# Kernel optimization log

Measured on AMD Instinct MI355X. Metric: run time of the kernel, lower is better.

Reference implementation:

```python
import jax, jax.numpy as jnp
import numpy as np

B, T, D = 16, 512, 256
HH = D // 2   # per-direction hidden of bidirectional GRU
G, Z, R, NA = 32, 8, 16, 18


def _gru_step(h, x, wih, whh, bih, bhh):
    # torch.nn.GRUCell math
    gi = x @ wih.T + bih
    gh = h @ whh.T + bhh
    ir, iz, inn = jnp.split(gi, 3, axis=-1)
    hr, hz, hn = jnp.split(gh, 3, axis=-1)
    r = jax.nn.sigmoid(ir + hr)
    z = jax.nn.sigmoid(iz + hz)
    n = jnp.tanh(inn + r * hn)
    return (1.0 - z) * n + z * h


def _gru_seq(x_tbd, wih, whh, bih, bhh):
    h0 = jnp.zeros((x_tbd.shape[1], whh.shape[1]), x_tbd.dtype)
    def step(h, x):
        h = _gru_step(h, x, wih, whh, bih, bhh)
        return h, h
    _, hs = jax.lax.scan(step, h0, x_tbd)
    return hs  # (T, B, H)


def setup_inputs() -> dict:
    key = jax.random.key(0)
    ks = jax.random.split(key, 26)
    rn = lambda k, s, sc: jax.random.normal(k, s, jnp.float32) * sc
    d = {
        'e_seq': rn(ks[0], (B, T, D), 1.0),
        'eps':   rn(ks[1], (B, T, Z), 1.0),
        # acausal bidirectional GRU (fwd + bwd cells)
        'wih_f': rn(ks[2], (3 * HH, D), D ** -0.5),  'whh_f': rn(ks[3], (3 * HH, HH), HH ** -0.5),
        'bih_f': jnp.zeros((3 * HH,)), 'bhh_f': jnp.zeros((3 * HH,)),
        'wih_b': rn(ks[4], (3 * HH, D), D ** -0.5),  'whh_b': rn(ks[5], (3 * HH, HH), HH ** -0.5),
        'bih_b': jnp.zeros((3 * HH,)), 'bhh_b': jnp.zeros((3 * HH,)),
        # controller encoder GRUCell(2D -> G) + heads
        'wih_e': rn(ks[6], (3 * G, 2 * D), (2 * D) ** -0.5), 'whh_e': rn(ks[7], (3 * G, G), G ** -0.5),
        'bih_e': jnp.zeros((3 * G,)), 'bhh_e': jnp.zeros((3 * G,)),
        'mu_w': rn(ks[8], (Z, G), G ** -0.5),  'mu_b': jnp.zeros((Z,)),
        'lv_w': rn(ks[9], (Z, G), G ** -0.5),  'lv_b': jnp.zeros((Z,)),
        # switching unit MLP (D+G+Z -> 64 -> 1)
        'sw1_w': rn(ks[10], (64, D + G + Z), (D + G + Z) ** -0.5), 'sw1_b': jnp.zeros((64,)),
        'sw2_w': rn(ks[11], (1, 64), 64 ** -0.5), 'sw2_b': jnp.zeros((1,)),
        # decoder hypernet (Z -> 32 -> 2*D*R)
        'dec1_w': rn(ks[12], (32, Z), Z ** -0.5), 'dec1_b': jnp.zeros((32,)),
        'dec2_w': rn(ks[13], (2 * D * R, 32), 32 ** -0.5), 'dec2_b': jnp.zeros((2 * D * R,)),
        # final norm + action head
        'ln_g': jnp.ones((D,)), 'ln_b': jnp.zeros((D,)),
        'head_w': rn(ks[14], (NA, D), D ** -0.5), 'head_b': jnp.zeros((NA,)),
    }
    return d


def _forward(e_seq, eps, wih_f, whh_f, bih_f, bhh_f, wih_b, whh_b, bih_b, bhh_b,
             wih_e, whh_e, bih_e, bhh_e, mu_w, mu_b, lv_w, lv_b,
             sw1_w, sw1_b, sw2_w, sw2_b, dec1_w, dec1_b, dec2_w, dec2_b,
             ln_g, ln_b, head_w, head_b):
    Bz, Tt, Dm = e_seq.shape
    e_tbd = jnp.swapaxes(e_seq, 0, 1)                      # (T, B, D)
    # AcausalEmbedder: bidirectional GRU
    fwd = _gru_seq(e_tbd, wih_f, whh_f, bih_f, bhh_f)
    bwd = _gru_seq(e_tbd[::-1], wih_b, whh_b, bih_b, bhh_b)[::-1]
    s_tbd = jnp.concatenate([fwd, bwd], axis=-1)           # (T, B, D)
    eps_tbd = jnp.swapaxes(eps, 0, 1)

    h0 = jnp.zeros((Bz, whh_e.shape[1]), e_seq.dtype)
    z0 = jnp.zeros((Bz, mu_w.shape[0]), e_seq.dtype)

    def step(carry, xs):
        h, z_prev = carry
        e_t, s_t, eps_t = xs
        h = _gru_step(h, jnp.concatenate([e_t, s_t], axis=-1), wih_e, whh_e, bih_e, bhh_e)
        mu = h @ mu_w.T + mu_b
        logvar = h @ lv_w.T + lv_b
        # switching unit uses updated h (causal)
        hid = jnp.tanh(jnp.concatenate([e_t, h, z_prev], axis=-1) @ sw1_w.T + sw1_b)
        beta = jax.nn.sigmoid(hid @ sw2_w.T + sw2_b)       # (B, 1)
        z = beta * (mu + jnp.exp(0.5 * logvar) * eps_t) + (1.0 - beta) * z_prev
        return (h, jax.lax.stop_gradient(z)), (mu, logvar, beta, z)

    _, (mu_t, lv_t, be_t, z_t) = jax.lax.scan(step, (h0, z0), (e_tbd, s_tbd, eps_tbd))
    mu_seq = jnp.swapaxes(mu_t, 0, 1)
    logvar_seq = jnp.swapaxes(lv_t, 0, 1)
    beta_seq = jnp.swapaxes(be_t, 0, 1)
    z_seq = jnp.swapaxes(z_t, 0, 1)                        # (B, T, Z)

    # ControllerDecoder: z -> (A, Bm); apply U = A @ Bm^T without materializing U
    hmid = jnp.tanh(z_seq @ dec1_w.T + dec1_b)
    ab = hmid @ dec2_w.T + dec2_b                          # (B, T, 2*D*R)
    DR = ab.shape[-1] // 2
    A = ab[..., :DR].reshape(Bz, Tt, Dm, -1)               # (B, T, D, R)
    Bm = ab[..., DR:].reshape(Bz, Tt, Dm, -1)
    tmp = jnp.einsum('btdr,btd->btr', Bm, e_seq)
    perturbed = e_seq + jnp.einsum('btdr,btr->btd', A, tmp)

    # final LayerNorm + action head on obs positions
    mean = perturbed.mean(-1, keepdims=True)
    var = perturbed.var(-1, keepdims=True)
    xn = (perturbed - mean) * jax.lax.rsqrt(var + 1e-5) * ln_g + ln_b
    logits = xn @ head_w.T + head_b                        # (B, T, NA)
    return logits, mu_seq, logvar_seq, beta_seq, z_seq


def reference(e_seq, eps, wih_f, whh_f, bih_f, bhh_f, wih_b, whh_b, bih_b, bhh_b,
              wih_e, whh_e, bih_e, bhh_e, mu_w, mu_b, lv_w, lv_b,
              sw1_w, sw1_b, sw2_w, sw2_b, dec1_w, dec1_b, dec2_w, dec2_b,
              ln_g, ln_b, head_w, head_b):
    return _forward(e_seq, eps, wih_f, whh_f, bih_f, bhh_f, wih_b, whh_b, bih_b, bhh_b,
                    wih_e, whh_e, bih_e, bhh_e, mu_w, mu_b, lv_w, lv_b,
                    sw1_w, sw1_b, sw2_w, sw2_b, dec1_w, dec1_b, dec2_w, dec2_b,
                    ln_g, ln_b, head_w, head_b)
```

## Files before the change

kernel.cpp:

```cpp
#include <hip/hip_runtime.h>

#define TT 512
#define BB 16
#define DD 256
#define HHH 128
#define GG 32
#define ZZ 8
#define RR_ 16
#define NAA 18

typedef _Float16 h2v __attribute__((ext_vector_type(2)));
typedef __attribute__((ext_vector_type(4))) float f4;
typedef __attribute__((ext_vector_type(4))) int i4;

__device__ __forceinline__ float sigmoid_(float x) { return 1.f / (1.f + __expf(-x)); }
__device__ __forceinline__ float tanh_(float x) { float e = __expf(2.f * x); return 1.f - 2.f / (e + 1.f); }
__device__ __forceinline__ float dot4(float4 a, float4 b) {
    return a.x * b.x + a.y * b.y + a.z * b.z + a.w * b.w;
}
__device__ __forceinline__ h2v u2h2(unsigned u) { union { unsigned u; h2v h; } c; c.u = u; return c.h; }

__device__ __forceinline__ void lds_barrier() {
    asm volatile("s_waitcnt lgkmcnt(0)" ::: "memory");
    __builtin_amdgcn_s_barrier();
}

#define AGPR_STORE(a, v) asm volatile("v_accvgpr_write_b32 %0, %1" : "=a"(a) : "v"(v))
#define AGPR_LOAD(v, a)  asm volatile("v_accvgpr_read_b32 %0, %1" : "=v"(v) : "a"(a))

template <int CTRL, int RM, int BM, bool BC>
__device__ __forceinline__ float dpp_add_f(float v) {
    return v + __int_as_float(__builtin_amdgcn_update_dpp(0, __float_as_int(v), CTRL, RM, BM, BC));
}
__device__ __forceinline__ float wave_sum_bcast(float p) {
    p = dpp_add_f<0x111, 0xf, 0xf, true>(p);
    p = dpp_add_f<0x112, 0xf, 0xf, true>(p);
    p = dpp_add_f<0x114, 0xf, 0xf, true>(p);
    p = dpp_add_f<0x118, 0xf, 0xf, true>(p);
    p = dpp_add_f<0x142, 0xa, 0xf, false>(p);
    p = dpp_add_f<0x143, 0xc, 0xf, false>(p);
    return __int_as_float(__builtin_amdgcn_readlane(__float_as_int(p), 63));
}
__device__ __forceinline__ float quad_sum(float v) {
    v = dpp_add_f<0xB1, 0xf, 0xf, true>(v);
    v = dpp_add_f<0x4E, 0xf, 0xf, true>(v);
    return v;
}

__global__ __launch_bounds__(256) void pack_w(
    const float* __restrict__ wf, const float* __restrict__ wb,
    const float* __restrict__ we,
    unsigned* __restrict__ pk, unsigned* __restrict__ pk_e)
{
    int i = blockIdx.x * 256 + threadIdx.x;
    if (i < 49152) {
        int dir = i / 24576; int r = i % 24576;
        int w = r / 3072;    int r2 = r % 3072;
        int T = r2 / 1024;   int r3 = r2 % 1024;
        int kt = r3 / 256;   int r4 = r3 % 256;
        int lane = r4 / 4;   int jd = r4 % 4;
        const float* wsrc = dir ? wb : wf;
        int row = T * 128 + 16 * w + (lane & 15);
        int k0 = kt * 32 + (lane >> 4) * 8 + 2 * jd;
        union { _Float16 h[2]; unsigned u; } c;
        c.h[0] = (_Float16)wsrc[row * 128 + k0];
        c.h[1] = (_Float16)wsrc[row * 128 + k0 + 1];
        pk[i] = c.u;
    } else if (i < 50688) {
        int ie = i - 49152;
        int s = ie / 384;  int rem = ie % 384;
        int k = rem / 12;  int e = rem % 12;
        int j = e / 4;     int m = e % 4;
        int row = j * 32 + k, k0 = 8 * s + 2 * m;
        union { _Float16 h[2]; unsigned u; } c;
        c.h[0] = (_Float16)we[row * 32 + k0];
        c.h[1] = (_Float16)we[row * 32 + k0 + 1];
        pk_e[ie] = c.u;
    }
}

__global__ __launch_bounds__(256) void gemm_k(
    const float* __restrict__ A, int K, const float* __restrict__ W, int ldw,
    const float* __restrict__ bias, float* __restrict__ Out, int ldout, int N, int accFlag)
{
    __shared__ float At[64][36];
    __shared__ float Wt[32][36];
    int row0 = blockIdx.x * 64, n0 = blockIdx.y * 32;
    int tid = threadIdx.x;
    int tx = tid & 15, ty = tid >> 4;
    float acc[4][2] = {};
    for (int k0 = 0; k0 < K; k0 += 32) {
        #pragma unroll
        for (int i = 0; i < 8; ++i) {
            int idx = tid + i * 256; int rr = idx >> 5, kk = idx & 31;
            At[rr][kk] = A[(size_t)(row0 + rr) * K + k0 + kk];
        }
        #pragma unroll
        for (int i = 0; i < 4; ++i) {
            int idx = tid + i * 256; int nn = idx >> 5, kk = idx & 31;
            Wt[nn][kk] = (n0 + nn < N) ? W[(size_t)(n0 + nn) * ldw + k0 + kk] : 0.f;
        }
        __syncthreads();
        #pragma unroll
        for (int kk = 0; kk < 32; kk += 4) {
            float4 w0 = *(const float4*)&Wt[tx][kk];
            float4 w1 = *(const float4*)&Wt[tx + 16][kk];
            #pragma unroll
            for (int rr = 0; rr < 4; ++rr) {
                float4 av = *(const float4*)&At[ty * 4 + rr][kk];
                acc[rr][0] += dot4(av, w0);
                acc[rr][1] += dot4(av, w1);
            }
        }
        __syncthreads();
    }
    #pragma unroll
    for (int cc = 0; cc < 2; ++cc) {
        int n = n0 + tx + cc * 16;
        if (n < N) {
            float badd = bias ? bias[n] : 0.f;
            #pragma unroll
            for (int rr = 0; rr < 4; ++rr) {
                int row = row0 + ty * 4 + rr;
                float v = acc[rr][cc] + badd;
                if (accFlag) Out[(size_t)row * ldout + n] += v;
                else         Out[(size_t)row * ldout + n] = v;
            }
        }
    }
}

__global__ __launch_bounds__(256) void gemm_gi(
    const float* __restrict__ A,
    const float* __restrict__ wf, const float* __restrict__ bf, float* __restrict__ of,
    const float* __restrict__ wb, const float* __restrict__ bb, float* __restrict__ ob)
{
    __shared__ float At[64][36];
    __shared__ float Wt[32][36];
    int y = blockIdx.y;
    const float* W; const float* bias; float* Out; int n0;
    if (y < 12) { W = wf; bias = bf; Out = of; n0 = y * 32; }
    else        { W = wb; bias = bb; Out = ob; n0 = (y - 12) * 32; }
    int row0 = blockIdx.x * 64;
    int tid = threadIdx.x;
    int tx = tid & 15, ty = tid >> 4;
    float acc[4][2] = {};
    for (int k0 = 0; k0 < 256; k0 += 32) {
        #pragma unroll
        for (int i = 0; i < 8; ++i) {
            int idx = tid + i * 256; int rr = idx >> 5, kk = idx & 31;
            At[rr][kk] = A[(size_t)(row0 + rr) * 256 + k0 + kk];
        }
        #pragma unroll
        for (int i = 0; i < 4; ++i) {
            int idx = tid + i * 256; int nn = idx >> 5, kk = idx & 31;
            Wt[nn][kk] = W[(size_t)(n0 + nn) * 256 + k0 + kk];
        }
        __syncthreads();
        #pragma unroll
        for (int kk = 0; kk < 32; kk += 4) {
            float4 w0 = *(const float4*)&Wt[tx][kk];
            float4 w1 = *(const float4*)&Wt[tx + 16][kk];
            #pragma unroll
            for (int rr = 0; rr < 4; ++rr) {
                float4 av = *(const float4*)&At[ty * 4 + rr][kk];
                acc[rr][0] += dot4(av, w0);
                acc[rr][1] += dot4(av, w1);
            }
        }
        __syncthreads();
    }
    #pragma unroll
    for (int cc = 0; cc < 2; ++cc) {
        int n = n0 + tx + cc * 16;
        float badd = bias[n];
        #pragma unroll
        for (int rr = 0; rr < 4; ++rr) {
            int row = row0 + ty * 4 + rr;
            Out[(size_t)row * 384 + n] = acc[rr][cc] + badd;
        }
    }
}

struct __align__(16) SmGru { _Float16 hb[2][128]; };
struct __align__(16) SmGemm { float At[64][36]; float Wt[32][36]; };
union __align__(16) SmU { SmGru g; SmGemm m; };

__device__ __forceinline__ void gemm_tile512(
    const float* __restrict__ A, int K, const float* __restrict__ W, int ldw,
    const float* __restrict__ bias, float* __restrict__ Out, int ldout, int N,
    int row0, int n0, SmGemm& sm)
{
    int tid = threadIdx.x;
    int tx = tid & 31, ty = tid >> 5;
    float acc[4] = {};
    for (int k0 = 0; k0 < K; k0 += 32) {
        #pragma unroll
        for (int i = 0; i < 4; ++i) {
            int idx = tid + i * 512; int rr = idx >> 5, kk = idx & 31;
            sm.At[rr][kk] = A[(size_t)(row0 + rr) * K + k0 + kk];
        }
        #pragma unroll
        for (int i = 0; i < 2; ++i) {
            int idx = tid + i * 512; int nn = idx >> 5, kk = idx & 31;
            sm.Wt[nn][kk] = (n0 + nn < N) ? W[(size_t)(n0 + nn) * ldw + k0 + kk] : 0.f;
        }
        __syncthreads();
        #pragma unroll
        for (int kk = 0; kk < 32; kk += 4) {
            float4 w0 = *(const float4*)&sm.Wt[tx][kk];
            #pragma unroll
            for (int rr = 0; rr < 4; ++rr) {
                float4 av = *(const float4*)&sm.At[ty * 4 + rr][kk];
                acc[rr] += dot4(av, w0);
            }
        }
        __syncthreads();
    }
    int n = n0 + tx;
    if (n < N) {
        float badd = bias ? bias[n] : 0.f;
        #pragma unroll
        for (int rr = 0; rr < 4; ++rr)
            Out[(size_t)(row0 + ty * 4 + rr) * ldout + n] = acc[rr] + badd;
    }
}

__global__ __launch_bounds__(512, 2) void gru_fused(
    const float* __restrict__ gi_f, const float* __restrict__ gi_b,
    const unsigned* __restrict__ pk,
    const float* __restrict__ bhh_f, const float* __restrict__ bhh_b,
    float* __restrict__ s_seq,
    const float* __restrict__ e,
    const float* __restrict__ wih_e, const float* __restrict__ bih_e, float* __restrict__ gie,
    const float* __restrict__ sw1_w, const float* __restrict__ sw1_b, float* __restrict__ swe)
{
    __shared__ SmU sm;
    int bx = blockIdx.x;
    if (bx >= 416) {
        int t = bx - 416;
        gemm_tile512(e, 256, sw1_w, 296, sw1_b, swe, 64, 64, (t & 127) * 64, (t >> 7) * 32, sm.m);
        return;
    }
    if (bx >= 32) {
        int t = bx - 32;
        gemm_tile512(e, 256, wih_e, 512, bih_e, gie, 96, 96, (t & 127) * 64, (t >> 7) * 32, sm.m);
        return;
    }

    int dir = bx >> 4, b = bx & 15;
    const float* gi  = dir ? gi_b  : gi_f;
    const float* bhh = dir ? bhh_b : bhh_f;
    int tid = threadIdx.x;
    int w = tid >> 6;
    int lane = tid & 63;
    int quad = lane >> 4;
    int c = lane & 15;
    int j = 16 * w + c;

    i4 bf[3][4];
    #pragma unroll
    for (int T = 0; T < 3; ++T)
        #pragma unroll
        for (int kt = 0; kt < 4; ++kt)
            bf[T][kt] = *(const i4*)(pk + (size_t)((((dir * 8 + w) * 3 + T) * 4 + kt) * 64 + lane) * 4);
    #pragma unroll
    for (int T = 0; T < 3; ++T)
        #pragma unroll
        for (int kt = 0; kt < 4; ++kt)
            asm volatile("" : "+a"(bf[T][kt]));

    if (tid < 128) sm.g.hb[0][tid] = (_Float16)0.f;

    float bhr = 0.f, bhz = 0.f, bhn = 0.f;
    float gra = 0.f, gza = 0.f, gna = 0.f;
    float grb = 0.f, gzb = 0.f, gnb = 0.f;
    float hreg = 0.f;
    if (lane < 16) {
        bhr = bhh[j]; bhz = bhh[128 + j]; bhn = bhh[256 + j];
        int t0 = dir ? 511 : 0;
        int t1 = dir ? 510 : 1;
        size_t p0 = (size_t)(b * TT + t0) * 384;
        size_t p1 = (size_t)(b * TT + t1) * 384;
        gra = gi[p0 + j]; gza = gi[p0 + 128 + j]; gna = gi[p0 + 256 + j];
        grb = gi[p1 + j]; gzb = gi[p1 + 128 + j]; gnb = gi[p1 + 256 + j];
    }
    __syncthreads();

    int cur = 0;
    auto body = [&](int step, float& gr, float& gz, float& gn) {
        i4 af[4];
        #pragma unroll
        for (int kt = 0; kt < 4; ++kt)
            af[kt] = *(const i4*)(&sm.g.hb[cur][kt * 32 + quad * 8]);
        f4 accr = {0.f, 0.f, 0.f, 0.f};
        f4 accz = {0.f, 0.f, 0.f, 0.f};
        f4 accn = {0.f, 0.f, 0.f, 0.f};
        asm volatile("s_nop 3");
        #pragma unroll
        for (int kt = 0; kt < 4; ++kt) {
            asm volatile("v_mfma_f32_16x16x32_f16 %0, %1, %2, %0" : "+v"(accr) : "v"(af[kt]), "a"(bf[0][kt]));
            asm volatile("v_mfma_f32_16x16x32_f16 %0, %1, %2, %0" : "+v"(accz) : "v"(af[kt]), "a"(bf[1][kt]));
            asm volatile("v_mfma_f32_16x16x32_f16 %0, %1, %2, %0" : "+v"(accn) : "v"(af[kt]), "a"(bf[2][kt]));
        }
        asm volatile("s_nop 7\n\ts_nop 7");
        if (lane < 16) {
            int t = dir ? (511 - step) : step;
            int p = b * TT + t;
            float r = sigmoid_(gr + bhr + accr[0]);
            float z = sigmoid_(gz + bhz + accz[0]);
            float n = tanh_(gn + r * (bhn + accn[0]));
            float hn = (1.f - z) * n + z * hreg;
            hreg = hn;
            sm.g.hb[cur ^ 1][j] = (_Float16)hn;
            s_seq[(size_t)p * 256 + dir * 128 + j] = hn;
            int s2 = step + 2;
            int tp = (s2 < 512) ? (dir ? (511 - s2) : s2) : t;
            size_t p2 = (size_t)(b * TT + tp) * 384;
            gr = gi[p2 + j]; gz = gi[p2 + 128 + j]; gn = gi[p2 + 256 + j];
        }
        lds_barrier();
        cur ^= 1;
    };

    for (int step = 0; step < 512; step += 2) {
        body(step,     gra, gza, gna);
        body(step + 1, grb, gzb, gnb);
    }
}

__global__ __launch_bounds__(256) void heads_k(
    const float* __restrict__ h_seq,
    const float* __restrict__ mu_w, const float* __restrict__ mu_b,
    const float* __restrict__ lv_w, const float* __restrict__ lv_b,
    const float* __restrict__ sw1_w,
    float* __restrict__ out_mu, float* __restrict__ out_lv, float* __restrict__ swe)
{
    __shared__ __align__(16) float Ah[64][32];
    int row0 = blockIdx.x * 64;
    int tid = threadIdx.x;
    #pragma unroll
    for (int i = 0; i < 8; ++i) {
        int idx = tid + i * 256; int rr = idx >> 5, kk = idx & 31;
        Ah[rr][kk] = h_seq[(size_t)(row0 + rr) * 32 + kk];
    }
    __syncthreads();
    int r = tid >> 2, g = tid & 3;
    const float4* av = (const float4*)Ah[r];
    float4 a[8];
    #pragma unroll
    for (int i = 0; i < 8; ++i) a[i] = av[i];
    int row = row0 + r;
    for (int c = 0; c < 20; ++c) {
        int n = g * 20 + c;
        const float* wrow;
        if (n < 8)       wrow = mu_w + n * 32;
        else if (n < 16) wrow = lv_w + (n - 8) * 32;
        else             wrow = sw1_w + (size_t)(n - 16) * 296 + 256;
        const float4* wv = (const float4*)wrow;
        float acc = 0.f;
        #pragma unroll
        for (int i = 0; i < 8; ++i) acc += dot4(wv[i], a[i]);
        if (n < 8)       out_mu[row * 8 + n] = acc + mu_b[n];
        else if (n < 16) out_lv[row * 8 + (n - 8)] = acc + lv_b[n - 8];
        else             swe[(size_t)row * 64 + (n - 16)] += acc;
    }
}

__global__ __launch_bounds__(128, 1) void ctrl_h_scan(
    const float* __restrict__ gie, const unsigned* __restrict__ pk_e,
    const float* __restrict__ bhh_e, float* __restrict__ h_seq)
{
    int b = blockIdx.x, tid = threadIdx.x;
    int k = tid >> 2;
    int s = tid & 3;

    unsigned ag[12];
    {
        const uint4* wp = (const uint4*)(pk_e + ((size_t)(s * 32) + k) * 12);
        #pragma unroll
        for (int i = 0; i < 3; ++i) {
            uint4 u = wp[i];
            AGPR_STORE(ag[4 * i + 0], u.x);
            AGPR_STORE(ag[4 * i + 1], u.y);
            AGPR_STORE(ag[4 * i + 2], u.z);
            AGPR_STORE(ag[4 * i + 3], u.w);
        }
    }

    __shared__ __align__(16) _Float16 hb[2][32];
    if (tid < 32) hb[0][tid] = (_Float16)0.f;

    int pbase = b * TT;
    float bhr = 0.f, bhz = 0.f, bhn = 0.f;
    float g1a = 0.f, g2a = 0.f, g3a = 0.f, g1b = 0.f, g2b = 0.f, g3b = 0.f;
    float hreg = 0.f;
    if (s == 0) {
        bhr = bhh_e[k]; bhz = bhh_e[32 + k]; bhn = bhh_e[64 + k];
        size_t p0 = (size_t)pbase * 96, p1 = (size_t)(pbase + 1) * 96;
        g1a = gie[p0 + k]; g2a = gie[p0 + 32 + k]; g3a = gie[p0 + 64 + k];
        g1b = gie[p1 + k]; g2b = gie[p1 + 32 + k]; g3b = gie[p1 + 64 + k];
    }
    __syncthreads();

    int cur = 0;
    auto body = [&](int t, float& g1, float& g2, float& g3) {
        const uint4* hv = (const uint4*)(&hb[cur][0]) + s;
        uint4 h4 = hv[0];
        unsigned hw[4] = { h4.x, h4.y, h4.z, h4.w };
        float a0 = 0.f, a1 = 0.f, a2 = 0.f;
        #pragma unroll
        for (int m = 0; m < 4; ++m) {
            unsigned w0, w1, w2;
            AGPR_LOAD(w0, ag[m]);
            AGPR_LOAD(w1, ag[4 + m]);
            AGPR_LOAD(w2, ag[8 + m]);
            h2v hh = u2h2(hw[m]);
            a0 = __builtin_amdgcn_fdot2(u2h2(w0), hh, a0, false);
            a1 = __builtin_amdgcn_fdot2(u2h2(w1), hh, a1, false);
            a2 = __builtin_amdgcn_fdot2(u2h2(w2), hh, a2, false);
        }
        a0 = quad_sum(a0);
        a1 = quad_sum(a1);
        a2 = quad_sum(a2);

        if (s == 0) {
            float r = sigmoid_(g1 + bhr + a0);
            float z = sigmoid_(g2 + bhz + a1);
            float n = tanh_(g3 + r * (bhn + a2));
            float hn = (1.f - z) * n + z * hreg;
            hreg = hn;
            hb[cur ^ 1][k] = (_Float16)hn;
            h_seq[(size_t)(pbase + t) * 32 + k] = hn;
            int t2 = (t + 2 < 512) ? t + 2 : t;
            size_t p2 = (size_t)(pbase + t2) * 96;
            g1 = gie[p2 + k]; g2 = gie[p2 + 32 + k]; g3 = gie[p2 + 64 + k];
        }
        lds_barrier();
        cur ^= 1;
    };

    for (int t = 0; t < 512; t += 2) {
        body(t,     g1a, g2a, g3a);
        body(t + 1, g1b, g2b, g3b);
    }
}

__global__ __launch_bounds__(64, 1) void ctrl_z_scan(
    const float* __restrict__ hid_pre, const float* __restrict__ sw1_w,
    const float* __restrict__ sw2_w, const float* __restrict__ sw2_b,
    const float* __restrict__ eps, const float* __restrict__ mu_o,
    const float* __restrict__ lv_o, float* __restrict__ beta_o, float* __restrict__ z_o)
{
    int b = blockIdx.x, q = threadIdx.x;
    float wz[8];
    #pragma unroll
    for (int x = 0; x < 8; ++x) wz[x] = sw1_w[(size_t)q * 296 + 288 + x];
    float w2 = sw2_w[q];
    float bb = sw2_b[0];
    float4 z03 = {0.f, 0.f, 0.f, 0.f}, z47 = {0.f, 0.f, 0.f, 0.f};
    int pbase = b * TT;

    auto loadcand = [&](int p, float4& c03, float4& c47) {
        float4 m0 = *(const float4*)(mu_o + p * 8);
        float4 m1 = *(const float4*)(mu_o + p * 8 + 4);
        float4 l0 = *(const float4*)(lv_o + p * 8);
        float4 l1 = *(const float4*)(lv_o + p * 8 + 4);
        float4 e0 = *(const float4*)(eps + p * 8);
        float4 e1 = *(const float4*)(eps + p * 8 + 4);
        c03 = make_float4(m0.x + __expf(0.5f * l0.x) * e0.x, m0.y + __expf(0.5f * l0.y) * e0.y,
                          m0.z + __expf(0.5f * l0.z) * e0.z, m0.w + __expf(0.5f * l0.w) * e0.w);
        c47 = make_float4(m1.x + __expf(0.5f * l1.x) * e1.x, m1.y + __expf(0.5f * l1.y) * e1.y,
                          m1.z + __expf(0.5f * l1.z) * e1.z, m1.w + __expf(0.5f * l1.w) * e1.w);
    };

    float hpa = hid_pre[(size_t)pbase * 64 + q];
    float hpb = hid_pre[(size_t)(pbase + 1) * 64 + q];
    float4 c03a, c47a, c03b, c47b;
    loadcand(pbase, c03a, c47a);
    loadcand(pbase + 1, c03b, c47b);

    auto body = [&](int t, float& hp, float4& c03, float4& c47) {
        int p = pbase + t;
        float a = hp
            + wz[0] * z03.x + wz[1] * z03.y + wz[2] * z03.z + wz[3] * z03.w
            + wz[4] * z47.x + wz[5] * z47.y + wz[6] * z47.z + wz[7] * z47.w;
        float hid = tanh_(a);
        float total = wave_sum_bcast(w2 * hid);
        float beta = sigmoid_(total + bb);
        float omb = 1.f - beta;
        z03.x = beta * c03.x + omb * z03.x;  z03.y = beta * c03.y + omb * z03.y;
        z03.z = beta * c03.z + omb * z03.z;  z03.w = beta * c03.w + omb * z03.w;
        z47.x = beta * c47.x + omb * z47.x;  z47.y = beta * c47.y + omb * z47.y;
        z47.z = beta * c47.z + omb * z47.z;  z47.w = beta * c47.w + omb * z47.w;
        if (q == 0) {
            *(float4*)(z_o + p * 8) = z03;
            *(float4*)(z_o + p * 8 + 4) = z47;
            beta_o[p] = beta;
        }
        int t2 = (t + 2 < 512) ? t + 2 : t;
        hp = hid_pre[(size_t)(pbase + t2) * 64 + q];
        loadcand(pbase + t2, c03, c47);
    };

    for (int t = 0; t < 512; t += 2) {
        body(t,     hpa, c03a, c47a);
        body(t + 1, hpb, c03b, c47b);
    }
}

__global__ __launch_bounds__(256, 3) void decoder_final(
    const float* __restrict__ e_seq, const float* __restrict__ z_o,
    const float* __restrict__ dec1_w, const float* __restrict__ dec1_b,
    const float* __restrict__ dec2_w, const float* __restrict__ dec2_b,
    const float* __restrict__ ln_g, const float* __restrict__ ln_b,
    const float* __restrict__ head_w, const float* __restrict__ head_b,
    float* __restrict__ logits)
{
    __shared__ __align__(16) float e_l[8][256];
    __shared__ __align__(16) float hmid[8][32];
    __shared__ float zl[8][8];
    __shared__ float tmpw[8][16];
    __shared__ __align__(16) float partb[2048];
    __shared__ float red1[8][16];
    __shared__ float red2[8][16];
    __shared__ float stats[8][2];
    int tid = threadIdx.x;
    int p0 = blockIdx.x * 8;

    {
        const float4* eg = (const float4*)(e_seq + (size_t)p0 * 256);
        float4* el4 = (float4*)&e_l[0][0];
        el4[tid] = eg[tid];
        el4[tid + 256] = eg[tid + 256];
        if (tid < 64) ((float*)zl)[tid] = z_o[p0 * 8 + tid];
    }
    __syncthreads();
    {
        int pp = tid >> 5, g = tid & 31;
        float a = dec1_b[g];
        #pragma unroll
        for (int x = 0; x < 8; ++x) a += dec1_w[g * 8 + x] * zl[pp][x];
        hmid[pp][g] = tanh_(a);
    }
    __syncthreads();
    {
        int r = tid & 15, dgrp = tid >> 4;
        float acc[8];
        #pragma unroll
        for (int pp = 0; pp < 8; ++pp) acc[pp] = 0.f;
        for (int iblk = 0; iblk < 8; ++iblk) {
            float4 wr[2][8]; float wb[2]; int dd[2];
            #pragma unroll
            for (int ii = 0; ii < 2; ++ii) {
                int d = dgrp + 16 * (iblk * 2 + ii);
                dd[ii] = d;
                int row = 4096 + d * 16 + r;
                const float4* wp = (const float4*)(dec2_w + (size_t)row * 32);
                #pragma unroll
                for (int g = 0; g < 8; ++g) wr[ii][g] = wp[g];
                wb[ii] = dec2_b[row];
            }
            #pragma unroll 1
            for (int pp = 0; pp < 8; ++pp) {
                const float4* hv = (const float4*)hmid[pp];
                float b0 = wb[0], b1 = wb[1];
                #pragma unroll
                for (int g = 0; g < 8; ++g) {
                    float4 hh = hv[g];
                    b0 += dot4(wr[0][g], hh);
                    b1 += dot4(wr[1][g], hh);
                }
                acc[pp] += b0 * e_l[pp][dd[0]] + b1 * e_l[pp][dd[1]];
            }
        }
        #pragma unroll
        for (int pp = 0; pp < 8; ++pp) partb[(pp * 16 + r) * 16 + dgrp] = acc[pp];
    }
    __syncthreads();
    if (tid < 128) {
        int pp = tid >> 4, rr = tid & 15;
        float s = 0.f;
        #pragma unroll
        for (int dg = 0; dg < 16; ++dg) s += partb[(pp * 16 + rr) * 16 + dg];
        tmpw[pp][rr] = s;
    }
    __syncthreads();
    {
        int d = tid;
        float po[8];
        #pragma unroll
        for (int pp = 0; pp < 8; ++pp) po[pp] = e_l[pp][d];
        for (int rblk = 0; rblk < 8; ++rblk) {
            float4 wr[2][8]; float wb[2];
            #pragma unroll
            for (int ii = 0; ii < 2; ++ii) {
                int row = d * 16 + rblk * 2 + ii;
                const float4* wp = (const float4*)(dec2_w + (size_t)row * 32);
                #pragma unroll
                for (int g = 0; g < 8; ++g) wr[ii][g] = wp[g];
                wb[ii] = dec2_b[row];
            }
            #pragma unroll 1
            for (int pp = 0; pp < 8; ++pp) {
                const float4* hv = (const float4*)hmid[pp];
                float a0 = wb[0], a1 = wb[1];
                #pragma unroll
                for (int g = 0; g < 8; ++g) {
                    float4 hh = hv[g];
                    a0 += dot4(wr[0][g], hh);
                    a1 += dot4(wr[1][g], hh);
                }
                po[pp] += a0 * tmpw[pp][rblk * 2] + a1 * tmpw[pp][rblk * 2 + 1];
            }
        }
        #pragma unroll
        for (int pp = 0; pp < 8; ++pp) partb[pp * 256 + d] = po[pp];
    }
    __syncthreads();
    if (tid < 128) {
        int pp = tid >> 4, c = tid & 15;
        float s = 0.f, s2 = 0.f;
        #pragma unroll
        for (int i = 0; i < 16; ++i) { float v = partb[pp * 256 + c * 16 + i]; s += v; s2 += v * v; }
        red1[pp][c] = s; red2[pp][c] = s2;
    }
    __syncthreads();
    if (tid < 8) {
        float s = 0.f, s2 = 0.f;
        #pragma unroll
        for (int c = 0; c < 16; ++c) { s += red1[tid][c]; s2 += red2[tid][c]; }
        float mean = s * (1.f / 256.f);
        float var = s2 * (1.f / 256.f) - mean * mean;
        stats[tid][0] = mean;
        stats[tid][1] = rsqrtf(var + 1e-5f);
    }
    __syncthreads();
    {
        int d = tid;
        float g = ln_g[d], bln = ln_b[d];
        #pragma unroll
        for (int pp = 0; pp < 8; ++pp) {
            float v = (partb[pp * 256 + d] - stats[pp][0]) * stats[pp][1];
            partb[pp * 256 + d] = v * g + bln;
        }
    }
    __syncthreads();
    if (tid < 144) {
        int pp = tid / 18, na = tid - pp * 18;
        float a = head_b[na];
        for (int d2 = 0; d2 < 256; ++d2)
            a += partb[pp * 256 + d2] * head_w[na * 256 + d2];
        logits[(size_t)(p0 + pp) * 18 + na] = a;
    }
}

extern "C" void kernel_launch(void* const* d_in, const int* in_sizes, int n_in,
                              void* d_out, int out_size, void* d_ws, size_t ws_size,
                              hipStream_t stream) {
    (void)in_sizes; (void)n_in; (void)out_size; (void)ws_size;
    const float* e     = (const float*)d_in[0];
    const float* eps   = (const float*)d_in[1];
    const float* wih_f = (const float*)d_in[2];
    const float* whh_f = (const float*)d_in[3];
    const float* bih_f = (const float*)d_in[4];
    const float* bhh_f = (const float*)d_in[5];
    const float* wih_b = (const float*)d_in[6];
    const float* whh_b = (const float*)d_in[7];
    const float* bih_b = (const float*)d_in[8];
    const float* bhh_b = (const float*)d_in[9];
    const float* wih_e = (const float*)d_in[10];
    const float* whh_e = (const float*)d_in[11];
    const float* bih_e = (const float*)d_in[12];
    const float* bhh_e = (const float*)d_in[13];
    const float* mu_w  = (const float*)d_in[14];
    const float* mu_b  = (const float*)d_in[15];
    const float* lv_w  = (const float*)d_in[16];
    const float* lv_b  = (const float*)d_in[17];
    const float* sw1_w = (const float*)d_in[18];
    const float* sw1_b = (const float*)d_in[19];
    const float* sw2_w = (const float*)d_in[20];
    const float* sw2_b = (const float*)d_in[21];
    const float* dec1_w = (const float*)d_in[22];
    const float* dec1_b = (const float*)d_in[23];
    const float* dec2_w = (const float*)d_in[24];
    const float* dec2_b = (const float*)d_in[25];
    const float* ln_g  = (const float*)d_in[26];
    const float* ln_b  = (const float*)d_in[27];
    const float* head_w = (const float*)d_in[28];
    const float* head_b = (const float*)d_in[29];

    float* ws    = (float*)d_ws;
    float* gi_f  = ws;
    float* gi_b  = gi_f + 3145728;
    float* gie   = gi_b + 3145728;
    float* swe   = gie + 786432;
    float* s_seq = swe + 524288;
    float* h_seq = s_seq + 2097152;
    unsigned* pk   = (unsigned*)(h_seq + 262144);
    unsigned* pk_e = pk + 49152;

    float* out       = (float*)d_out;
    float* out_logit = out;
    float* out_mu    = out + 147456;
    float* out_lv    = out + 212992;
    float* out_beta  = out + 278528;
    float* out_z     = out + 286720;

    pack_w<<<198, 256, 0, stream>>>(whh_f, whh_b, whh_e, pk, pk_e);
    gemm_gi<<<dim3(128, 24), 256, 0, stream>>>(e, wih_f, bih_f, gi_f, wih_b, bih_b, gi_b);
    gru_fused<<<672, 512, 0, stream>>>(gi_f, gi_b, pk, bhh_f, bhh_b, s_seq,
                                       e, wih_e, bih_e, gie, sw1_w, sw1_b, swe);
    gemm_k<<<dim3(128, 3), 256, 0, stream>>>(s_seq, 256, wih_e + 256, 512, nullptr, gie, 96, 96, 1);
    ctrl_h_scan<<<16, 128, 0, stream>>>(gie, pk_e, bhh_e, h_seq);
    heads_k<<<128, 256, 0, stream>>>(h_seq, mu_w, mu_b, lv_w, lv_b, sw1_w, out_mu, out_lv, swe);
    ctrl_z_scan<<<16, 64, 0, stream>>>(swe, sw1_w, sw2_w, sw2_b, eps, out_mu, out_lv, out_beta, out_z);
    decoder_final<<<1024, 256, 0, stream>>>(e, out_z, dec1_w, dec1_b, dec2_w, dec2_b,
                                            ln_g, ln_b, head_w, head_b, out_logit);
}
```

Before: 1.097 ms.

## Fuse controller GRU scan, heads and switch scan into one pipelined kernel

Replaces the separate ctrl_h_scan, heads_k and ctrl_z_scan launches with one kernel per batch row. Wave 0 runs the controller GRU recurrence and wave 1 runs the mu/logvar heads and the switching z-scan one step behind, passing h through LDS, so the two serial scans overlap and the h_seq round trip through global memory goes away. The bidirectional GRU MFMA chain is also split into two independent accumulator chains so consecutive MFMAs do not wait on each other. The costs are more per-thread registers and a barrier every step between the two waves.

```diff
diff --git a/kernel.cpp b/kernel.cpp
--- a/kernel.cpp
+++ b/kernel.cpp
@@ -24,9 +24,6 @@
     asm volatile("s_waitcnt lgkmcnt(0)" ::: "memory");
     __builtin_amdgcn_s_barrier();
 }
-
-#define AGPR_STORE(a, v) asm volatile("v_accvgpr_write_b32 %0, %1" : "=a"(a) : "v"(v))
-#define AGPR_LOAD(v, a)  asm volatile("v_accvgpr_read_b32 %0, %1" : "=v"(v) : "a"(a))
 
 template <int CTRL, int RM, int BM, bool BC>
 __device__ __forceinline__ float dpp_add_f(float v) {
@@ -293,23 +290,32 @@
         #pragma unroll
         for (int kt = 0; kt < 4; ++kt)
             af[kt] = *(const i4*)(&sm.g.hb[cur][kt * 32 + quad * 8]);
-        f4 accr = {0.f, 0.f, 0.f, 0.f};
-        f4 accz = {0.f, 0.f, 0.f, 0.f};
-        f4 accn = {0.f, 0.f, 0.f, 0.f};
+        f4 accrA = {0.f, 0.f, 0.f, 0.f}, accrB = {0.f, 0.f, 0.f, 0.f};
+        f4 acczA = {0.f, 0.f, 0.f, 0.f}, acczB = {0.f, 0.f, 0.f, 0.f};
+        f4 accnA = {0.f, 0.f, 0.f, 0.f}, accnB = {0.f, 0.f, 0.f, 0.f};
         asm volatile("s_nop 3");
-        #pragma unroll
-        for (int kt = 0; kt < 4; ++kt) {
-            asm volatile("v_mfma_f32_16x16x32_f16 %0, %1, %2, %0" : "+v"(accr) : "v"(af[kt]), "a"(bf[0][kt]));
-            asm volatile("v_mfma_f32_16x16x32_f16 %0, %1, %2, %0" : "+v"(accz) : "v"(af[kt]), "a"(bf[1][kt]));
-            asm volatile("v_mfma_f32_16x16x32_f16 %0, %1, %2, %0" : "+v"(accn) : "v"(af[kt]), "a"(bf[2][kt]));
-        }
+        asm volatile("v_mfma_f32_16x16x32_f16 %0, %1, %2, %0" : "+v"(accrA) : "v"(af[0]), "a"(bf[0][0]));
+        asm volatile("v_mfma_f32_16x16x32_f16 %0, %1, %2, %0" : "+v"(acczA) : "v"(af[0]), "a"(bf[1][0]));
+        asm volatile("v_mfma_f32_16x16x32_f16 %0, %1, %2, %0" : "+v"(accnA) : "v"(af[0]), "a"(bf[2][0]));
+        asm volatile("v_mfma_f32_16x16x32_f16 %0, %1, %2, %0" : "+v"(accrB) : "v"(af[2]), "a"(bf[0][2]));
+        asm volatile("v_mfma_f32_16x16x32_f16 %0, %1, %2, %0" : "+v"(acczB) : "v"(af[2]), "a"(bf[1][2]));
+        asm volatile("v_mfma_f32_16x16x32_f16 %0, %1, %2, %0" : "+v"(accnB) : "v"(af[2]), "a"(bf[2][2]));
+        asm volatile("v_mfma_f32_16x16x32_f16 %0, %1, %2, %0" : "+v"(accrA) : "v"(af[1]), "a"(bf[0][1]));
+        asm volatile("v_mfma_f32_16x16x32_f16 %0, %1, %2, %0" : "+v"(acczA) : "v"(af[1]), "a"(bf[1][1]));
+        asm volatile("v_mfma_f32_16x16x32_f16 %0, %1, %2, %0" : "+v"(accnA) : "v"(af[1]), "a"(bf[2][1]));
+        asm volatile("v_mfma_f32_16x16x32_f16 %0, %1, %2, %0" : "+v"(accrB) : "v"(af[3]), "a"(bf[0][3]));
+        asm volatile("v_mfma_f32_16x16x32_f16 %0, %1, %2, %0" : "+v"(acczB) : "v"(af[3]), "a"(bf[1][3]));
+        asm volatile("v_mfma_f32_16x16x32_f16 %0, %1, %2, %0" : "+v"(accnB) : "v"(af[3]), "a"(bf[2][3]));
         asm volatile("s_nop 7\n\ts_nop 7");
         if (lane < 16) {
             int t = dir ? (511 - step) : step;
             int p = b * TT + t;
-            float r = sigmoid_(gr + bhr + accr[0]);
-            float z = sigmoid_(gz + bhz + accz[0]);
-            float n = tanh_(gn + r * (bhn + accn[0]));
+            float ar = accrA[0] + accrB[0];
+            float az = acczA[0] + acczB[0];
+            float an = accnA[0] + accnB[0];
+            float r = sigmoid_(gr + bhr + ar);
+            float z = sigmoid_(gz + bhz + az);
+            float n = tanh_(gn + r * (bhn + an));
             float hn = (1.f - z) * n + z * hreg;
             hreg = hn;
             sm.g.hb[cur ^ 1][j] = (_Float16)hn;
@@ -329,184 +335,172 @@
     }
 }
 
-__global__ __launch_bounds__(256) void heads_k(
-    const float* __restrict__ h_seq,
+__global__ __launch_bounds__(128, 1) void ctrl_fused(
+    const float* __restrict__ gie, const unsigned* __restrict__ pk_e,
+    const float* __restrict__ bhh_e,
     const float* __restrict__ mu_w, const float* __restrict__ mu_b,
     const float* __restrict__ lv_w, const float* __restrict__ lv_b,
-    const float* __restrict__ sw1_w,
-    float* __restrict__ out_mu, float* __restrict__ out_lv, float* __restrict__ swe)
+    const float* __restrict__ sw1_w, const float* __restrict__ sw2_w,
+    const float* __restrict__ sw2_b,
+    const float* __restrict__ swe,
+    const float* __restrict__ eps,
+    float* __restrict__ out_mu, float* __restrict__ out_lv,
+    float* __restrict__ beta_o, float* __restrict__ z_o)
 {
-    __shared__ __align__(16) float Ah[64][32];
-    int row0 = blockIdx.x * 64;
+    int b = blockIdx.x;
     int tid = threadIdx.x;
-    #pragma unroll
-    for (int i = 0; i < 8; ++i) {
-        int idx = tid + i * 256; int rr = idx >> 5, kk = idx & 31;
-        Ah[rr][kk] = h_seq[(size_t)(row0 + rr) * 32 + kk];
-    }
-    __syncthreads();
-    int r = tid >> 2, g = tid & 3;
-    const float4* av = (const float4*)Ah[r];
-    float4 a[8];
-    #pragma unroll
-    for (int i = 0; i < 8; ++i) a[i] = av[i];
-    int row = row0 + r;
-    for (int c = 0; c < 20; ++c) {
-        int n = g * 20 + c;
-        const float* wrow;
-        if (n < 8)       wrow = mu_w + n * 32;
-        else if (n < 16) wrow = lv_w + (n - 8) * 32;
-        else             wrow = sw1_w + (size_t)(n - 16) * 296 + 256;
-        const float4* wv = (const float4*)wrow;
-        float acc = 0.f;
-        #pragma unroll
-        for (int i = 0; i < 8; ++i) acc += dot4(wv[i], a[i]);
-        if (n < 8)       out_mu[row * 8 + n] = acc + mu_b[n];
-        else if (n < 16) out_lv[row * 8 + (n - 8)] = acc + lv_b[n - 8];
-        else             swe[(size_t)row * 64 + (n - 16)] += acc;
-    }
-}
-
-__global__ __launch_bounds__(128, 1) void ctrl_h_scan(
-    const float* __restrict__ gie, const unsigned* __restrict__ pk_e,
-    const float* __restrict__ bhh_e, float* __restrict__ h_seq)
-{
-    int b = blockIdx.x, tid = threadIdx.x;
-    int k = tid >> 2;
-    int s = tid & 3;
-
-    unsigned ag[12];
-    {
-        const uint4* wp = (const uint4*)(pk_e + ((size_t)(s * 32) + k) * 12);
-        #pragma unroll
-        for (int i = 0; i < 3; ++i) {
-            uint4 u = wp[i];
-            AGPR_STORE(ag[4 * i + 0], u.x);
-            AGPR_STORE(ag[4 * i + 1], u.y);
-            AGPR_STORE(ag[4 * i + 2], u.z);
-            AGPR_STORE(ag[4 * i + 3], u.w);
-        }
-    }
+    int wid = tid >> 6;
+    int lane = tid & 63;
+    int pbase = b * TT;
 
     __shared__ __align__(16) _Float16 hb[2][32];
-    if (tid < 32) hb[0][tid] = (_Float16)0.f;
-
-    int pbase = b * TT;
-    float bhr = 0.f, bhz = 0.f, bhn = 0.f;
+    __shared__ __align__(16) float    hf[2][32];
+    __shared__ __align__(16) float    zc[8];
+
+    int k = lane >> 1, s2 = lane & 1;
+    unsigned wg[24];
+    float bhr = 0.f, bhz = 0.f, bhn = 0.f, hreg = 0.f;
     float g1a = 0.f, g2a = 0.f, g3a = 0.f, g1b = 0.f, g2b = 0.f, g3b = 0.f;
-    float hreg = 0.f;
-    if (s == 0) {
-        bhr = bhh_e[k]; bhz = bhh_e[32 + k]; bhn = bhh_e[64 + k];
-        size_t p0 = (size_t)pbase * 96, p1 = (size_t)(pbase + 1) * 96;
-        g1a = gie[p0 + k]; g2a = gie[p0 + 32 + k]; g3a = gie[p0 + 64 + k];
-        g1b = gie[p1 + k]; g2b = gie[p1 + 32 + k]; g3b = gie[p1 + 64 + k];
+    if (wid == 0) {
+        #pragma unroll
+        for (int ss = 0; ss < 2; ++ss) {
+            const uint4* wp = (const uint4*)(pk_e + ((size_t)((2 * s2 + ss) * 32) + k) * 12);
+            #pragma unroll
+            for (int i = 0; i < 3; ++i) {
+                uint4 u = wp[i];
+                wg[12 * ss + 4 * i + 0] = u.x;
+                wg[12 * ss + 4 * i + 1] = u.y;
+                wg[12 * ss + 4 * i + 2] = u.z;
+                wg[12 * ss + 4 * i + 3] = u.w;
+            }
+        }
+        if (tid < 32) hb[0][tid] = (_Float16)0.f;
+        if (s2 == 0) {
+            bhr = bhh_e[k]; bhz = bhh_e[32 + k]; bhn = bhh_e[64 + k];
+            size_t p0 = (size_t)pbase * 96, p1 = (size_t)(pbase + 1) * 96;
+            g1a = gie[p0 + k]; g2a = gie[p0 + 32 + k]; g3a = gie[p0 + 64 + k];
+            g1b = gie[p1 + k]; g2b = gie[p1 + 32 + k]; g3b = gie[p1 + 64 + k];
+        }
+    }
+
+    int q = lane;
+    int x = lane >> 3, kind = (lane >> 2) & 1, s = lane & 3;
+    float swh[32], wz[8], mlw[8];
+    float w2 = 0.f, sb2 = 0.f, mlb = 0.f;
+    float zreg[8] = {0.f, 0.f, 0.f, 0.f, 0.f, 0.f, 0.f, 0.f};
+    float hpa = 0.f, hpb = 0.f, epa = 0.f, epb = 0.f;
+    if (wid == 1) {
+        #pragma unroll
+        for (int kk = 0; kk < 32; ++kk) swh[kk] = sw1_w[(size_t)q * 296 + 256 + kk];
+        #pragma unroll
+        for (int xx = 0; xx < 8; ++xx) wz[xx] = sw1_w[(size_t)q * 296 + 288 + xx];
+        w2 = sw2_w[q];
+        sb2 = sw2_b[0];
+        const float* mw = kind ? lv_w : mu_w;
+        #pragma unroll
+        for (int m = 0; m < 8; ++m) mlw[m] = mw[x * 32 + 8 * s + m];
+        mlb = kind ? lv_b[x] : mu_b[x];
+        hpa = swe[(size_t)pbase * 64 + q];
+        hpb = swe[(size_t)(pbase + 1) * 64 + q];
+        epa = eps[(size_t)pbase * 8 + x];
+        epb = eps[(size_t)(pbase + 1) * 8 + x];
     }
     __syncthreads();
 
     int cur = 0;
-    auto body = [&](int t, float& g1, float& g2, float& g3) {
-        const uint4* hv = (const uint4*)(&hb[cur][0]) + s;
-        uint4 h4 = hv[0];
-        unsigned hw[4] = { h4.x, h4.y, h4.z, h4.w };
-        float a0 = 0.f, a1 = 0.f, a2 = 0.f;
+
+    auto prod = [&](int t, float& g1, float& g2, float& g3) {
+        const uint4* hv = (const uint4*)(&hb[cur][16 * s2]);
+        uint4 hA = hv[0], hB = hv[1];
+        unsigned hw[8] = {hA.x, hA.y, hA.z, hA.w, hB.x, hB.y, hB.z, hB.w};
+        float a0 = 0.f, a1 = 0.f, a2 = 0.f, c0 = 0.f, c1 = 0.f, c2 = 0.f;
         #pragma unroll
         for (int m = 0; m < 4; ++m) {
-            unsigned w0, w1, w2;
-            AGPR_LOAD(w0, ag[m]);
-            AGPR_LOAD(w1, ag[4 + m]);
-            AGPR_LOAD(w2, ag[8 + m]);
-            h2v hh = u2h2(hw[m]);
-            a0 = __builtin_amdgcn_fdot2(u2h2(w0), hh, a0, false);
-            a1 = __builtin_amdgcn_fdot2(u2h2(w1), hh, a1, false);
-            a2 = __builtin_amdgcn_fdot2(u2h2(w2), hh, a2, false);
-        }
-        a0 = quad_sum(a0);
-        a1 = quad_sum(a1);
-        a2 = quad_sum(a2);
-
-        if (s == 0) {
+            a0 = __builtin_amdgcn_fdot2(u2h2(wg[m]),      u2h2(hw[m]),     a0, false);
+            a1 = __builtin_amdgcn_fdot2(u2h2(wg[4 + m]),  u2h2(hw[m]),     a1, false);
+            a2 = __builtin_amdgcn_fdot2(u2h2(wg[8 + m]),  u2h2(hw[m]),     a2, false);
+            c0 = __builtin_amdgcn_fdot2(u2h2(wg[12 + m]), u2h2(hw[4 + m]), c0, false);
+            c1 = __builtin_amdgcn_fdot2(u2h2(wg[16 + m]), u2h2(hw[4 + m]), c1, false);
+            c2 = __builtin_amdgcn_fdot2(u2h2(wg[20 + m]), u2h2(hw[4 + m]), c2, false);
+        }
+        a0 += c0; a1 += c1; a2 += c2;
+        a0 = dpp_add_f<0xB1, 0xf, 0xf, true>(a0);
+        a1 = dpp_add_f<0xB1, 0xf, 0xf, true>(a1);
+        a2 = dpp_add_f<0xB1, 0xf, 0xf, true>(a2);
+        if (s2 == 0) {
             float r = sigmoid_(g1 + bhr + a0);
             float z = sigmoid_(g2 + bhz + a1);
             float n = tanh_(g3 + r * (bhn + a2));
             float hn = (1.f - z) * n + z * hreg;
             hreg = hn;
             hb[cur ^ 1][k] = (_Float16)hn;
-            h_seq[(size_t)(pbase + t) * 32 + k] = hn;
+            hf[cur ^ 1][k] = hn;
             int t2 = (t + 2 < 512) ? t + 2 : t;
             size_t p2 = (size_t)(pbase + t2) * 96;
             g1 = gie[p2 + k]; g2 = gie[p2 + 32 + k]; g3 = gie[p2 + 64 + k];
         }
+    };
+
+    auto cons = [&](int t, float& hp, float& ep) {
+        const float4* hv4 = (const float4*)(&hf[cur][0]);
+        float4 h4[8];
+        #pragma unroll
+        for (int i = 0; i < 8; ++i) h4[i] = hv4[i];
+        float a = hp;
+        #pragma unroll
+        for (int xx = 0; xx < 8; ++xx) a += wz[xx] * zreg[xx];
+        #pragma unroll
+        for (int i = 0; i < 8; ++i) {
+            a += swh[4 * i]     * h4[i].x;
+            a += swh[4 * i + 1] * h4[i].y;
+            a += swh[4 * i + 2] * h4[i].z;
+            a += swh[4 * i + 3] * h4[i].w;
+        }
+        float hid = tanh_(a);
+        float beta = sigmoid_(wave_sum_bcast(w2 * hid) + sb2);
+        float4 hs0 = *(const float4*)(&hf[cur][8 * s]);
+        float4 hs1 = *(const float4*)(&hf[cur][8 * s + 4]);
+        float pacc = mlw[0] * hs0.x + mlw[1] * hs0.y + mlw[2] * hs0.z + mlw[3] * hs0.w
+                   + mlw[4] * hs1.x + mlw[5] * hs1.y + mlw[6] * hs1.z + mlw[7] * hs1.w;
+        pacc = quad_sum(pacc);
+        float v = pacc + mlb;
+        float other = __int_as_float(__builtin_amdgcn_ds_swizzle(__float_as_int(v), 0x101F));
+        float muv = kind ? other : v;
+        float lvv = kind ? v : other;
+        float cand = muv + __expf(0.5f * lvv) * ep;
+        if ((lane & 7) == 0) zc[x] = cand;
+        asm volatile("s_waitcnt lgkmcnt(0)" ::: "memory");
+        float4 cz0 = *(const float4*)&zc[0];
+        float4 cz1 = *(const float4*)&zc[4];
+        float omb = 1.f - beta;
+        zreg[0] = beta * cz0.x + omb * zreg[0]; zreg[1] = beta * cz0.y + omb * zreg[1];
+        zreg[2] = beta * cz0.z + omb * zreg[2]; zreg[3] = beta * cz0.w + omb * zreg[3];
+        zreg[4] = beta * cz1.x + omb * zreg[4]; zreg[5] = beta * cz1.y + omb * zreg[5];
+        zreg[6] = beta * cz1.z + omb * zreg[6]; zreg[7] = beta * cz1.w + omb * zreg[7];
+        int p = pbase + t;
+        if (lane == 0) {
+            beta_o[p] = beta;
+            *(float4*)(z_o + (size_t)p * 8)     = make_float4(zreg[0], zreg[1], zreg[2], zreg[3]);
+            *(float4*)(z_o + (size_t)p * 8 + 4) = make_float4(zreg[4], zreg[5], zreg[6], zreg[7]);
+        }
+        if ((lane & 7) == 0) out_mu[(size_t)p * 8 + x] = muv;
+        if ((lane & 7) == 4) out_lv[(size_t)p * 8 + x] = lvv;
+        int t2 = (t + 2 < 512) ? t + 2 : t;
+        hp = swe[(size_t)(pbase + t2) * 64 + q];
+        ep = eps[(size_t)(pbase + t2) * 8 + x];
+    };
+
+    for (int it = 0; it < 512; it += 2) {
+        if (wid == 0) prod(it, g1a, g2a, g3a);
+        else if (it > 0) cons(it - 1, hpb, epb);
         lds_barrier();
         cur ^= 1;
-    };
-
-    for (int t = 0; t < 512; t += 2) {
-        body(t,     g1a, g2a, g3a);
-        body(t + 1, g1b, g2b, g3b);
-    }
-}
-
-__global__ __launch_bounds__(64, 1) void ctrl_z_scan(
-    const float* __restrict__ hid_pre, const float* __restrict__ sw1_w,
-    const float* __restrict__ sw2_w, const float* __restrict__ sw2_b,
-    const float* __restrict__ eps, const float* __restrict__ mu_o,
-    const float* __restrict__ lv_o, float* __restrict__ beta_o, float* __restrict__ z_o)
-{
-    int b = blockIdx.x, q = threadIdx.x;
-    float wz[8];
-    #pragma unroll
-    for (int x = 0; x < 8; ++x) wz[x] = sw1_w[(size_t)q * 296 + 288 + x];
-    float w2 = sw2_w[q];
-    float bb = sw2_b[0];
-    float4 z03 = {0.f, 0.f, 0.f, 0.f}, z47 = {0.f, 0.f, 0.f, 0.f};
-    int pbase = b * TT;
-
-    auto loadcand = [&](int p, float4& c03, float4& c47) {
-        float4 m0 = *(const float4*)(mu_o + p * 8);
-        float4 m1 = *(const float4*)(mu_o + p * 8 + 4);
-        float4 l0 = *(const float4*)(lv_o + p * 8);
-        float4 l1 = *(const float4*)(lv_o + p * 8 + 4);
-        float4 e0 = *(const float4*)(eps + p * 8);
-        float4 e1 = *(const float4*)(eps + p * 8 + 4);
-        c03 = make_float4(m0.x + __expf(0.5f * l0.x) * e0.x, m0.y + __expf(0.5f * l0.y) * e0.y,
-                          m0.z + __expf(0.5f * l0.z) * e0.z, m0.w + __expf(0.5f * l0.w) * e0.w);
-        c47 = make_float4(m1.x + __expf(0.5f * l1.x) * e1.x, m1.y + __expf(0.5f * l1.y) * e1.y,
-                          m1.z + __expf(0.5f * l1.z) * e1.z, m1.w + __expf(0.5f * l1.w) * e1.w);
-    };
-
-    float hpa = hid_pre[(size_t)pbase * 64 + q];
-    float hpb = hid_pre[(size_t)(pbase + 1) * 64 + q];
-    float4 c03a, c47a, c03b, c47b;
-    loadcand(pbase, c03a, c47a);
-    loadcand(pbase + 1, c03b, c47b);
-
-    auto body = [&](int t, float& hp, float4& c03, float4& c47) {
-        int p = pbase + t;
-        float a = hp
-            + wz[0] * z03.x + wz[1] * z03.y + wz[2] * z03.z + wz[3] * z03.w
-            + wz[4] * z47.x + wz[5] * z47.y + wz[6] * z47.z + wz[7] * z47.w;
-        float hid = tanh_(a);
-        float total = wave_sum_bcast(w2 * hid);
-        float beta = sigmoid_(total + bb);
-        float omb = 1.f - beta;
-        z03.x = beta * c03.x + omb * z03.x;  z03.y = beta * c03.y + omb * z03.y;
-        z03.z = beta * c03.z + omb * z03.z;  z03.w = beta * c03.w + omb * z03.w;
-        z47.x = beta * c47.x + omb * z47.x;  z47.y = beta * c47.y + omb * z47.y;
-        z47.z = beta * c47.z + omb * z47.z;  z47.w = beta * c47.w + omb * z47.w;
-        if (q == 0) {
-            *(float4*)(z_o + p * 8) = z03;
-            *(float4*)(z_o + p * 8 + 4) = z47;
-            beta_o[p] = beta;
-        }
-        int t2 = (t + 2 < 512) ? t + 2 : t;
-        hp = hid_pre[(size_t)(pbase + t2) * 64 + q];
-        loadcand(pbase + t2, c03, c47);
-    };
-
-    for (int t = 0; t < 512; t += 2) {
-        body(t,     hpa, c03a, c47a);
-        body(t + 1, hpb, c03b, c47b);
-    }
+        if (wid == 0) prod(it + 1, g1b, g2b, g3b);
+        else cons(it, hpa, epa);
+        lds_barrier();
+        cur ^= 1;
+    }
+    if (wid == 1) cons(511, hpb, epb);
 }
 
 __global__ __launch_bounds__(256, 3) void decoder_final(
@@ -699,6 +693,7 @@
     float* h_seq = s_seq + 2097152;
     unsigned* pk   = (unsigned*)(h_seq + 262144);
     unsigned* pk_e = pk + 49152;
+    (void)h_seq;
 
     float* out       = (float*)d_out;
     float* out_logit = out;
@@ -712,9 +707,9 @@
     gru_fused<<<672, 512, 0, stream>>>(gi_f, gi_b, pk, bhh_f, bhh_b, s_seq,
                                        e, wih_e, bih_e, gie, sw1_w, sw1_b, swe);
     gemm_k<<<dim3(128, 3), 256, 0, stream>>>(s_seq, 256, wih_e + 256, 512, nullptr, gie, 96, 96, 1);
-    ctrl_h_scan<<<16, 128, 0, stream>>>(gie, pk_e, bhh_e, h_seq);
-    heads_k<<<128, 256, 0, stream>>>(h_seq, mu_w, mu_b, lv_w, lv_b, sw1_w, out_mu, out_lv, swe);
-    ctrl_z_scan<<<16, 64, 0, stream>>>(swe, sw1_w, sw2_w, sw2_b, eps, out_mu, out_lv, out_beta, out_z);
+    ctrl_fused<<<16, 128, 0, stream>>>(gie, pk_e, bhh_e, mu_w, mu_b, lv_w, lv_b,
+                                       sw1_w, sw2_w, sw2_b, swe, eps,
+                                       out_mu, out_lv, out_beta, out_z);
     decoder_final<<<1024, 256, 0, stream>>>(e, out_z, dec1_w, dec1_b, dec2_w, dec2_b,
                                             ln_g, ln_b, head_w, head_b, out_logit);
 }
```

After: 1.005 ms. 1.09x faster.
